# Performance work log

Measured on AMD Instinct MI355X. Metric: run time of the kernel, lower is better.

The kernel has to match this reference:

```python
import jax, jax.numpy as jnp
import numpy as np

B, H, W, C = 1, 256, 256, 256  # pooled feature map, NHWC
OH, OW = 2 * H, 2 * W          # unpooled output spatial dims


def setup_inputs() -> dict:
    key = jax.random.key(0)
    val = jax.random.normal(key, (B, H, W, C), dtype=jnp.float32)
    # Canonical argmax indices: each pooled element maps to the top-left
    # corner of its 2x2 window in the flattened [OH, OW, C] output.
    h = jnp.arange(H, dtype=jnp.int32)[:, None, None]   # [H,1,1]
    w = jnp.arange(W, dtype=jnp.int32)[None, :, None]   # [1,W,1]
    c = jnp.arange(C, dtype=jnp.int32)[None, None, :]   # [1,1,C]
    index = ((2 * h) * OW + (2 * w)) * C + c            # [H,W,C]
    index = jnp.broadcast_to(index, (B, H, W, C))
    return {"val": val, "index": index}


def reference(val, index):
    # tf.scatter_nd into a flat buffer of size OH*OW*C (duplicates sum),
    # then reshape to [-1, OH, OW, C].
    flat = jnp.zeros((OH * OW * C,), dtype=val.dtype)
    flat = flat.at[index.reshape(-1)].add(val.reshape(-1))
    return flat.reshape(-1, OH, OW, C)
```

## Files before the change

kernel.cpp:

```cpp
#include <hip/hip_runtime.h>


typedef float  f32x4 __attribute__((ext_vector_type(4)));
typedef int    i32x4 __attribute__((ext_vector_type(4)));

__global__ __launch_bounds__(256) void unpool_outcentric_kernel(
    const float* __restrict__ val,
    const int*   __restrict__ idx,
    float*       __restrict__ out,
    int nq)
{
    const int tid = blockIdx.x * blockDim.x + threadIdx.x;
    if (tid >= nq) return;

    f32x4* o = reinterpret_cast<f32x4*>(out);
    const f32x4 z = (f32x4)(0.f);

    const int c4 = tid & 63;
    const int ow = (tid >> 6) & 511;
    const int oh = tid >> 15;

    if ((oh | ow) & 1) {
        __builtin_nontemporal_store(z, o + tid);
        return;
    }

    const int qin = ((oh >> 1) << 14) + ((ow >> 1) << 6) + c4;
    const f32x4 v  = __builtin_nontemporal_load(reinterpret_cast<const f32x4*>(val) + qin);
    const i32x4 id = __builtin_nontemporal_load(reinterpret_cast<const i32x4*>(idx) + qin);

    const int p = tid << 2;
    if (__builtin_expect(id.x == p && id.y == p + 1 && id.z == p + 2 && id.w == p + 3, 1)) {
        __builtin_nontemporal_store(v, o + tid);
    } else {
        __builtin_nontemporal_store(z, o + tid);
        atomicAdd(out + id.x, v.x);
        atomicAdd(out + id.y, v.y);
        atomicAdd(out + id.z, v.z);
        atomicAdd(out + id.w, v.w);
    }
}

extern "C" void kernel_launch(void* const* d_in, const int* in_sizes, int n_in,
                              void* d_out, int out_size, void* d_ws, size_t ws_size,
                              hipStream_t stream) {
    const float* val = (const float*)d_in[0];
    const int*   idx = (const int*)d_in[1];
    float* out = (float*)d_out;

    const int n  = in_sizes[0];
    const int nq = n;
    const int block = 256;
    const int grid  = (nq + block - 1) / block;
    unpool_outcentric_kernel<<<grid, block, 0, stream>>>(val, idx, out, nq);
}
```

Measured before the change: 336.3 us.

## Split unpool into separate zero-fill and input-centric scatter kernels

Replaces the single output-centric kernel with two kernels. The first zero-fills the whole output buffer with plain vector stores, each thread writing four float4s. The second walks the pooled input: for each quad it checks the expected canonical index and writes it directly, falling back to atomics otherwise. This removes the per-output-thread parity branching and the gathered input reads, at the cost of writing the populated quarter of the output twice and adding a kernel launch.

```diff
diff --git a/kernel.cpp b/kernel.cpp
--- a/kernel.cpp
+++ b/kernel.cpp
@@ -4,36 +4,38 @@
 typedef float  f32x4 __attribute__((ext_vector_type(4)));
 typedef int    i32x4 __attribute__((ext_vector_type(4)));
 
-__global__ __launch_bounds__(256) void unpool_outcentric_kernel(
+__global__ __launch_bounds__(256) void zero_fill_kernel(float* __restrict__ out)
+{
+    f32x4* o = reinterpret_cast<f32x4*>(out);
+    const f32x4 z = (f32x4)(0.f);
+    const int base = blockIdx.x * 1024 + threadIdx.x;
+    #pragma unroll
+    for (int k = 0; k < 4; ++k)
+        o[base + k * 256] = z;
+}
+
+__global__ __launch_bounds__(256) void scatter_canonical_kernel(
     const float* __restrict__ val,
     const int*   __restrict__ idx,
     float*       __restrict__ out,
-    int nq)
+    int niq)
 {
     const int tid = blockIdx.x * blockDim.x + threadIdx.x;
-    if (tid >= nq) return;
+    if (tid >= niq) return;
 
-    f32x4* o = reinterpret_cast<f32x4*>(out);
-    const f32x4 z = (f32x4)(0.f);
+    const f32x4 v  = __builtin_nontemporal_load(reinterpret_cast<const f32x4*>(val) + tid);
+    const i32x4 id = __builtin_nontemporal_load(reinterpret_cast<const i32x4*>(idx) + tid);
 
     const int c4 = tid & 63;
-    const int ow = (tid >> 6) & 511;
-    const int oh = tid >> 15;
+    const int w  = (tid >> 6) & 255;
+    const int h  = tid >> 14;
 
-    if ((oh | ow) & 1) {
-        __builtin_nontemporal_store(z, o + tid);
-        return;
-    }
+    const int p00 = h * 262144 + w * 512 + c4 * 4;
 
-    const int qin = ((oh >> 1) << 14) + ((ow >> 1) << 6) + c4;
-    const f32x4 v  = __builtin_nontemporal_load(reinterpret_cast<const f32x4*>(val) + qin);
-    const i32x4 id = __builtin_nontemporal_load(reinterpret_cast<const i32x4*>(idx) + qin);
-
-    const int p = tid << 2;
-    if (__builtin_expect(id.x == p && id.y == p + 1 && id.z == p + 2 && id.w == p + 3, 1)) {
-        __builtin_nontemporal_store(v, o + tid);
+    if (__builtin_expect(id.x == p00     && id.y == p00 + 1 &&
+                         id.z == p00 + 2 && id.w == p00 + 3, 1)) {
+        reinterpret_cast<f32x4*>(out)[p00 >> 2] = v;
     } else {
-        __builtin_nontemporal_store(z, o + tid);
         atomicAdd(out + id.x, v.x);
         atomicAdd(out + id.y, v.y);
         atomicAdd(out + id.z, v.z);
@@ -48,9 +50,13 @@
     const int*   idx = (const int*)d_in[1];
     float* out = (float*)d_out;
 
-    const int n  = in_sizes[0];
-    const int nq = n;
+    const int n   = in_sizes[0];
+    const int nq  = n;
+    const int niq = n / 4;
+
+    zero_fill_kernel<<<nq / 1024, 256, 0, stream>>>(out);
+
     const int block = 256;
-    const int grid  = (nq + block - 1) / block;
-    unpool_outcentric_kernel<<<grid, block, 0, stream>>>(val, idx, out, nq);
+    const int grid  = (niq + block - 1) / block;
+    scatter_canonical_kernel<<<grid, block, 0, stream>>>(val, idx, out, niq);
 }
```

Result: slower. 350.7 us (+4.3%).
